# Kernel tuning notes

Hardware: AMD Instinct MI355X
Metric: run time of the kernel (lower is better)

The kernel has to match this reference:

```python
import jax, jax.numpy as jnp
import numpy as np

EPS = 1e-12  # matches torch F.normalize eps


def setup_inputs() -> dict:
    key = jax.random.key(0)
    k1, k2 = jax.random.split(key)
    N, D, K = 262144, 128, 512
    embeddings = jax.random.normal(k1, (N, D), dtype=jnp.float32)
    init_centroids = jax.random.normal(k2, (K, D), dtype=jnp.float32)
    return {"embeddings": embeddings, "init_centroids": init_centroids, "num_iters": 5}


def _kmeans_iter(centroids, embeddings, K):
    # [N, K] similarity, hard assignment by argmax (k-means E-step with dot-product metric)
    dots = jnp.matmul(embeddings, centroids.T)
    assign = jnp.argmax(dots, axis=1)  # [N] int32
    # M-step: per-cluster sum + counts (replaces CPU dict-of-lists + python loop)
    emb_sums = jax.ops.segment_sum(embeddings, assign, num_segments=K)  # [K, D]
    counts = jax.ops.segment_sum(jnp.ones(embeddings.shape[0], dtype=embeddings.dtype),
                                 assign, num_segments=K)  # [K]
    # only update clusters with members (mask = counts > 0), keep old centroid otherwise
    new_c = jnp.where(counts[:, None] > 0,
                      emb_sums / jnp.maximum(counts, 1.0)[:, None],
                      centroids)
    # F.normalize(dim=1, p=2) applied to ALL centroids
    norm = jnp.maximum(jnp.linalg.norm(new_c, axis=1, keepdims=True), EPS)
    return new_c / norm, assign


def reference(embeddings, init_centroids, num_iters):
    K = init_centroids.shape[0]
    centroids = init_centroids
    assign = jnp.zeros(embeddings.shape[0], dtype=jnp.int32)
    for _ in range(num_iters):  # small static iteration count (k-means iters)
        centroids, assign = _kmeans_iter(centroids, embeddings, K)
    return assign, centroids
```

## Files before the change

### kernel.cpp

```cpp
#include <hip/hip_runtime.h>

#define NN 262144
#define DD 128
#define KK 512
#define NITER 5

#define SKH 136

#define SE 132
#define SC 260
#define SS 129

#define DELTA 2e-3f

#define WS_A16_BYTES   (NN * 2)
#define WS_SUMS_OFF    (WS_A16_BYTES)
#define WS_CNTS_OFF    (WS_SUMS_OFF + 2048 * DD * 4)
#define WS_NEEDED      (WS_CNTS_OFF + 2048 * 4)
#define WS_CH_OFF      (WS_SUMS_OFF + NN)
#define WS_CL_OFF      (WS_CH_OFF + KK * DD * 2)

using s8    = __attribute__((ext_vector_type(8))) short;
using f32x4 = __attribute__((ext_vector_type(4))) float;

__device__ __forceinline__ unsigned f2bf(float x) {
    unsigned u = __float_as_uint(x);
    return (u + 0x7fffu + ((u >> 16) & 1u)) >> 16;
}

__device__ __forceinline__ void split4(float4 v, uint2& h, uint2& s) {
    unsigned hx = f2bf(v.x), hy = f2bf(v.y), hz = f2bf(v.z), hw = f2bf(v.w);
    float rx = v.x - __uint_as_float(hx << 16);
    float ry = v.y - __uint_as_float(hy << 16);
    float rz = v.z - __uint_as_float(hz << 16);
    float rw = v.w - __uint_as_float(hw << 16);
    unsigned lx = f2bf(rx), ly = f2bf(ry), lz = f2bf(rz), lw = f2bf(rw);
    h.x = hx | (hy << 16); h.y = hz | (hw << 16);
    s.x = lx | (ly << 16); s.y = lz | (lw << 16);
}

__global__ __launch_bounds__(256) void split_c_kernel(
    const float* __restrict__ C, unsigned short* __restrict__ CH,
    unsigned short* __restrict__ CL)
{
    int idx = blockIdx.x * 256 + threadIdx.x;
    int col = idx >> 5;
    int k4  = (idx & 31) << 2;
    float4 v = *(const float4*)&C[(size_t)col * DD + k4];
    uint2 h, s;
    split4(v, h, s);
    int group = (col >> 4) * 4 + (k4 >> 5);
    int inner = ((k4 >> 3) & 3) * 16 + (col & 15);
    int off   = group * 512 + inner * 8 + (k4 & 7);
    *(uint2*)&CH[off] = h;
    *(uint2*)&CL[off] = s;
}

__global__ __launch_bounds__(256, 2) void assign_kernel(
    const float* __restrict__ E,
    const unsigned short* __restrict__ CH, const unsigned short* __restrict__ CL,
    int* __restrict__ assignv, unsigned short* __restrict__ assign16,
    unsigned char* __restrict__ flags)
{
    __shared__ unsigned short lds[2 * 128 * SKH];
    unsigned short* EH = lds;
    unsigned short* EL = lds + 128 * SKH;

    const int tid = threadIdx.x;
    const int l   = tid & 63;
    const int wid = tid >> 6;
    const int wr  = wid >> 1;
    const int wc  = wid & 1;
    const int c   = l & 15;
    const int g   = l >> 4;
    const int r0  = blockIdx.x * 128;

#pragma unroll
    for (int it = 0; it < 16; ++it) {
        int idx = it * 256 + tid;
        int row = idx >> 5;
        int k4  = (idx & 31) << 2;
        float4 v = *(const float4*)&E[(size_t)(r0 + row) * DD + k4];
        uint2 h, s;
        split4(v, h, s);
        *(uint2*)&EH[row * SKH + k4] = h;
        *(uint2*)&EL[row * SKH + k4] = s;
    }
    __syncthreads();

    float bv[16], sv[16];
    int   bk[16];
#pragma unroll
    for (int i = 0; i < 16; ++i) { bv[i] = -3.4e38f; sv[i] = -3.4e38f; bk[i] = 0; }

    const int aoff0 = (wr * 64 + c) * SKH + g * 8;
    const int bbase = wc * 16 * 512 + l * 8;

    s8 bh[2][4], bl[2][4];
#pragma unroll
    for (int cf = 0; cf < 4; ++cf) {
        int off = bbase + (cf * 4) * 512;
        bh[0][cf] = *(const s8*)&CH[off];
        bl[0][cf] = *(const s8*)&CL[off];
    }

    f32x4 acc[4][4];

#pragma unroll
    for (int t = 0; t < 16; ++t) {
        const int cc  = t >> 2, kc = t & 3;
        const int cur = t & 1,  nxt = cur ^ 1;

        if (kc == 0) {
#pragma unroll
            for (int rf = 0; rf < 4; ++rf)
#pragma unroll
                for (int cf = 0; cf < 4; ++cf)
                    acc[rf][cf] = (f32x4){0.f, 0.f, 0.f, 0.f};
        }

        if (t < 15) {
            const int t1 = t + 1, cc1 = t1 >> 2, kc1 = t1 & 3;
#pragma unroll
            for (int cf = 0; cf < 4; ++cf) {
                int off = bbase + (cc1 * 32 + cf * 4 + kc1) * 512;
                bh[nxt][cf] = *(const s8*)&CH[off];
                bl[nxt][cf] = *(const s8*)&CL[off];
            }
        }

        s8 ah[4], al[4];
#pragma unroll
        for (int rf = 0; rf < 4; ++rf) {
            int off = aoff0 + rf * 16 * SKH + kc * 32;
            ah[rf] = *(const s8*)&EH[off];
            al[rf] = *(const s8*)&EL[off];
        }

#pragma unroll
        for (int rf = 0; rf < 4; ++rf)
#pragma unroll
            for (int cf = 0; cf < 4; ++cf) {
                acc[rf][cf] = __builtin_amdgcn_mfma_f32_16x16x32_bf16(
                    ah[rf], bh[cur][cf], acc[rf][cf], 0, 0, 0);
                acc[rf][cf] = __builtin_amdgcn_mfma_f32_16x16x32_bf16(
                    ah[rf], bl[cur][cf], acc[rf][cf], 0, 0, 0);
                acc[rf][cf] = __builtin_amdgcn_mfma_f32_16x16x32_bf16(
                    al[rf], bh[cur][cf], acc[rf][cf], 0, 0, 0);
            }

        if (kc == 3) {
            const int kbase = cc * 128 + wc * 64 + c;
#pragma unroll
            for (int rf = 0; rf < 4; ++rf)
#pragma unroll
                for (int i = 0; i < 4; ++i) {
                    const int sidx = rf * 4 + i;
#pragma unroll
                    for (int cf = 0; cf < 4; ++cf) {
                        float v = acc[rf][cf][i];
                        int  kg = kbase + cf * 16;
                        if (v > bv[sidx]) { sv[sidx] = bv[sidx]; bv[sidx] = v; bk[sidx] = kg; }
                        else              { sv[sidx] = fmaxf(sv[sidx], v); }
                    }
                }
        }
    }

#pragma unroll
    for (int s = 0; s < 16; ++s) {
        float v1 = bv[s], v2 = sv[s]; int k1 = bk[s];
#pragma unroll
        for (int m = 1; m <= 8; m <<= 1) {
            float ov = __shfl_xor(v1, m, 64);
            float os = __shfl_xor(v2, m, 64);
            int   ok = __shfl_xor(k1, m, 64);
            if (ov > v1) { v2 = fmaxf(v1, os); v1 = ov; k1 = ok; }
            else         { v2 = fmaxf(v2, ov); }
        }
        bv[s] = v1; sv[s] = v2; bk[s] = k1;
    }

    __syncthreads();
    float* mv = (float*)lds;
    int*   mk = (int*)lds + 256;
    float* ms = (float*)lds + 512;
    if (c == 0) {
#pragma unroll
        for (int rf = 0; rf < 4; ++rf)
#pragma unroll
            for (int i = 0; i < 4; ++i) {
                int row = wr * 64 + rf * 16 + g * 4 + i;
                mv[wc * 128 + row] = bv[rf * 4 + i];
                mk[wc * 128 + row] = bk[rf * 4 + i];
                ms[wc * 128 + row] = sv[rf * 4 + i];
            }
    }
    __syncthreads();
    if (tid < 128) {
        float v1 = mv[tid], v2 = ms[tid]; int k1 = mk[tid];
        float ov = mv[128 + tid], os = ms[128 + tid]; int ok = mk[128 + tid];
        if (ov > v1) { v2 = fmaxf(v1, os); v1 = ov; k1 = ok; }
        else         { v2 = fmaxf(v2, ov); }
        assignv[r0 + tid] = k1;
        assign16[r0 + tid] = (unsigned short)k1;
        flags[r0 + tid] = (v1 - v2 < DELTA) ? 1 : 0;
    }
}

__global__ __launch_bounds__(256) void rescue_kernel(
    const float* __restrict__ E, const float* __restrict__ C,
    const unsigned char* __restrict__ flags,
    int* __restrict__ assignv, unsigned short* __restrict__ assign16)
{
    __shared__ int   rows[128];
    __shared__ int   nf;
    __shared__ float ev[DD];
    __shared__ float rv[4];
    __shared__ int   rk[4];

    const int tid  = threadIdx.x;
    const int base = blockIdx.x * 128;

    if (tid == 0) nf = 0;
    __syncthreads();
    if (tid < 128 && flags[base + tid]) {
        int p = atomicAdd(&nf, 1);
        rows[p] = base + tid;
    }
    __syncthreads();
    const int n = nf;
    if (n == 0) return;

    for (int i = 0; i < n; ++i) {
        const int row = rows[i];
        if (tid < 32)
            *(float4*)&ev[tid * 4] = *(const float4*)&E[(size_t)row * DD + tid * 4];
        __syncthreads();

        float d0 = 0.f, d1 = 0.f;
        for (int q = 0; q < 32; ++q) {
            float4 e4 = *(const float4*)&ev[q * 4];
            float4 c0 = *(const float4*)&C[(size_t)tid * DD + q * 4];
            float4 c1 = *(const float4*)&C[(size_t)(tid + 256) * DD + q * 4];
            d0 = fmaf(e4.x, c0.x, d0); d0 = fmaf(e4.y, c0.y, d0);
            d0 = fmaf(e4.z, c0.z, d0); d0 = fmaf(e4.w, c0.w, d0);
            d1 = fmaf(e4.x, c1.x, d1); d1 = fmaf(e4.y, c1.y, d1);
            d1 = fmaf(e4.z, c1.z, d1); d1 = fmaf(e4.w, c1.w, d1);
        }
        float v = (d0 >= d1) ? d0 : d1;
        int   k = (d0 >= d1) ? tid : tid + 256;
#pragma unroll
        for (int m = 1; m <= 32; m <<= 1) {
            float ov = __shfl_xor(v, m, 64);
            int   ok = __shfl_xor(k, m, 64);
            if (ov > v || (ov == v && ok < k)) { v = ov; k = ok; }
        }
        if ((tid & 63) == 0) { rv[tid >> 6] = v; rk[tid >> 6] = k; }
        __syncthreads();
        if (tid == 0) {
            float bv2 = rv[0]; int bk2 = rk[0];
#pragma unroll
            for (int w = 1; w < 4; ++w)
                if (rv[w] > bv2 || (rv[w] == bv2 && rk[w] < bk2)) { bv2 = rv[w]; bk2 = rk[w]; }
            assignv[row] = bk2;
            assign16[row] = (unsigned short)bk2;
        }
        __syncthreads();
    }
}

__global__ __launch_bounds__(256, 2) void assign_valu_kernel(
    const float* __restrict__ E, const float* __restrict__ C,
    int* __restrict__ assignv, unsigned short* __restrict__ assign16)
{
    __shared__ float smem[32 * SE + 32 * SC];
    float* ET = smem;
    float* CT = smem + 32 * SE;
    float* sval = smem;
    int*   sidx = ((int*)smem) + 32 * SS;

    const int tid = threadIdx.x;
    const int tx  = tid & 31;
    const int ty  = tid >> 5;
    const int r0  = blockIdx.x * 128;

    float bbv = 0.f;
    int   bbk = 0;

    for (int chunk = 0; chunk < 2; ++chunk) {
        const int k0 = chunk * 256;
        float acc[16][8];
#pragma unroll
        for (int i = 0; i < 16; ++i)
#pragma unroll
            for (int j = 0; j < 8; ++j) acc[i][j] = 0.f;

        for (int sub = 0; sub < 4; ++sub) {
            const int d0 = sub * 32;
            __syncthreads();
#pragma unroll
            for (int it = 0; it < 4; ++it) {
                int idx = tid + it * 256;
                int r = idx >> 3, q = idx & 7;
                float4 v = *(const float4*)&E[(r0 + r) * DD + d0 + q * 4];
                ET[(q * 4 + 0) * SE + r] = v.x;
                ET[(q * 4 + 1) * SE + r] = v.y;
                ET[(q * 4 + 2) * SE + r] = v.z;
                ET[(q * 4 + 3) * SE + r] = v.w;
            }
#pragma unroll
            for (int it = 0; it < 8; ++it) {
                int idx = tid + it * 256;
                int k = idx >> 3, q = idx & 7;
                float4 v = *(const float4*)&C[(k0 + k) * DD + d0 + q * 4];
                CT[(q * 4 + 0) * SC + k] = v.x;
                CT[(q * 4 + 1) * SC + k] = v.y;
                CT[(q * 4 + 2) * SC + k] = v.z;
                CT[(q * 4 + 3) * SC + k] = v.w;
            }
            __syncthreads();
#pragma unroll 4
            for (int d = 0; d < 32; ++d) {
                float4 a0 = *(const float4*)&ET[d * SE + ty * 16];
                float4 a1 = *(const float4*)&ET[d * SE + ty * 16 + 4];
                float4 a2 = *(const float4*)&ET[d * SE + ty * 16 + 8];
                float4 a3 = *(const float4*)&ET[d * SE + ty * 16 + 12];
                float4 b0 = *(const float4*)&CT[d * SC + tx * 4];
                float4 b1 = *(const float4*)&CT[d * SC + 128 + tx * 4];
                float ra[16] = {a0.x, a0.y, a0.z, a0.w, a1.x, a1.y, a1.z, a1.w,
                                a2.x, a2.y, a2.z, a2.w, a3.x, a3.y, a3.z, a3.w};
                float rb[8]  = {b0.x, b0.y, b0.z, b0.w, b1.x, b1.y, b1.z, b1.w};
#pragma unroll
                for (int i = 0; i < 16; ++i)
#pragma unroll
                    for (int j = 0; j < 8; ++j)
                        acc[i][j] = fmaf(ra[i], rb[j], acc[i][j]);
            }
        }
        __syncthreads();

#pragma unroll
        for (int i = 0; i < 16; ++i) {
            float bv = acc[i][0]; int bj = 0;
#pragma unroll
            for (int j = 1; j < 8; ++j)
                if (acc[i][j] > bv) { bv = acc[i][j]; bj = j; }
            int row = ty * 16 + i;
            int gk = k0 + ((bj < 4) ? (tx * 4 + bj) : (128 + tx * 4 + (bj - 4)));
            sval[tx * SS + row] = bv;
            sidx[tx * SS + row] = gk;
        }
        __syncthreads();
        if (tid < 128) {
            float bv = sval[tid]; int bi = sidx[tid];
            for (int t = 1; t < 32; ++t) {
                float v = sval[t * SS + tid];
                int   x = sidx[t * SS + tid];
                if (v > bv || (v == bv && x < bi)) { bv = v; bi = x; }
            }
            if (chunk == 0 || bv > bbv || (bv == bbv && bi < bbk)) {
                bbv = bv; bbk = bi;
            }
        }
    }
    if (tid < 128) {
        assignv[r0 + tid] = bbk;
        if (assign16) assign16[r0 + tid] = (unsigned short)bbk;
    }
}

__global__ __launch_bounds__(256) void update_partial_kernel(
    const float* __restrict__ E, const unsigned short* __restrict__ assign16,
    float* __restrict__ ws_sums, int* __restrict__ ws_cnts)
{
    const int b   = blockIdx.x;
    const int k   = b >> 2;
    const int qtr = b & 3;

    __shared__ float acc[4][DD];
    __shared__ int   cnts[4];

    const int tid  = threadIdx.x;
    const int w    = tid >> 6;
    const int lane = tid & 63;

    float a0 = 0.f, a1 = 0.f;
    int cnt = 0;
    const int wbase = qtr * (NN / 4) + w * (NN / 16);

    for (int it = 0; it < (NN / 16) / 512; ++it) {
        const int off = wbase + it * 512;
        uint4 p = *(const uint4*)&assign16[off + lane * 8];
        unsigned v[4] = {p.x, p.y, p.z, p.w};
#pragma unroll
        for (int h = 0; h < 4; ++h) {
            int lo = (int)(v[h] & 0xffffu);
            int hi = (int)(v[h] >> 16);
            unsigned long long mlo = __ballot(lo == k);
            unsigned long long mhi = __ballot(hi == k);
            cnt += (int)__popcll(mlo) + (int)__popcll(mhi);
            while (mlo) {
                int b2 = __ffsll((long long)mlo) - 1; mlo &= mlo - 1;
                int row = off + b2 * 8 + h * 2;
                float2 e = *(const float2*)&E[(size_t)row * DD + lane * 2];
                a0 += e.x; a1 += e.y;
            }
            while (mhi) {
                int b2 = __ffsll((long long)mhi) - 1; mhi &= mhi - 1;
                int row = off + b2 * 8 + h * 2 + 1;
                float2 e = *(const float2*)&E[(size_t)row * DD + lane * 2];
                a0 += e.x; a1 += e.y;
            }
        }
    }
    acc[w][lane * 2]     = a0;
    acc[w][lane * 2 + 1] = a1;
    if (lane == 0) cnts[w] = cnt;
    __syncthreads();
    if (tid < DD)
        ws_sums[(size_t)b * DD + tid] = acc[0][tid] + acc[1][tid] + acc[2][tid] + acc[3][tid];
    if (tid == 0)
        ws_cnts[b] = cnts[0] + cnts[1] + cnts[2] + cnts[3];
}

__global__ __launch_bounds__(128) void update_combine_kernel(
    const float* __restrict__ ws_sums, const int* __restrict__ ws_cnts,
    float* __restrict__ C)
{
    const int k = blockIdx.x, t = threadIdx.x;
    __shared__ float red[2];
    const int w = t >> 6, lane = t & 63;

    float s = ws_sums[(size_t)(4 * k + 0) * DD + t]
            + ws_sums[(size_t)(4 * k + 1) * DD + t]
            + ws_sums[(size_t)(4 * k + 2) * DD + t]
            + ws_sums[(size_t)(4 * k + 3) * DD + t];
    int cnt = ws_cnts[4 * k] + ws_cnts[4 * k + 1] + ws_cnts[4 * k + 2] + ws_cnts[4 * k + 3];
    float m = (cnt > 0) ? s / (float)cnt : C[k * DD + t];

    float sq = m * m;
#pragma unroll
    for (int o = 32; o > 0; o >>= 1) sq += __shfl_down(sq, o, 64);
    if (lane == 0) red[w] = sq;
    __syncthreads();
    float nrm = fmaxf(sqrtf(red[0] + red[1]), 1e-12f);
    C[k * DD + t] = m / nrm;
}

__global__ __launch_bounds__(256) void update_kernel(
    const float* __restrict__ E, const int* __restrict__ assignv,
    float* __restrict__ C)
{
    const int k = blockIdx.x;
    __shared__ float acc[4][DD];
    __shared__ int   cnts[4];
    __shared__ float red[4];

    const int tid  = threadIdx.x;
    const int w    = tid >> 6;
    const int lane = tid & 63;

    float a0 = 0.f, a1 = 0.f;
    int cnt = 0;
    const int per_wave = NN / 4;
    const int base = w * per_wave;

    for (int it = 0; it < per_wave / 256; ++it) {
        const int off = base + it * 256;
        int4 as = *(const int4*)&assignv[off + lane * 4];
        int av[4] = {as.x, as.y, as.z, as.w};
#pragma unroll
        for (int ci = 0; ci < 4; ++ci) {
            unsigned long long m = __ballot(av[ci] == k);
            cnt += (int)__popcll(m);
            while (m) {
                int b = __ffsll((long long)m) - 1;
                m &= m - 1;
                int r = off + b * 4 + ci;
                float2 v = *(const float2*)&E[r * DD + lane * 2];
                a0 += v.x; a1 += v.y;
            }
        }
    }
    acc[w][lane * 2]     = a0;
    acc[w][lane * 2 + 1] = a1;
    if (lane == 0) cnts[w] = cnt;
    __syncthreads();

    float m = 0.f;
    const int ctot = cnts[0] + cnts[1] + cnts[2] + cnts[3];
    if (tid < DD) {
        float s = acc[0][tid] + acc[1][tid] + acc[2][tid] + acc[3][tid];
        m = (ctot > 0) ? s / (float)ctot : C[k * DD + tid];
    }
    float sq = m * m;
#pragma unroll
    for (int o = 32; o > 0; o >>= 1) sq += __shfl_down(sq, o, 64);
    if (lane == 0) red[w] = sq;
    __syncthreads();
    if (tid < DD) {
        float nrm = fmaxf(sqrtf(red[0] + red[1]), 1e-12f);
        C[k * DD + tid] = m / nrm;
    }
}

__global__ void finalize_kernel(float* __restrict__ out)
{
    int i = blockIdx.x * 256 + threadIdx.x;
    if (i < NN) {
        int a = ((const int*)out)[i];
        out[i] = (float)a;
    }
}

extern "C" void kernel_launch(void* const* d_in, const int* in_sizes, int n_in,
                              void* d_out, int out_size, void* d_ws, size_t ws_size,
                              hipStream_t stream)
{
    (void)in_sizes; (void)n_in; (void)out_size;

    const float* E  = (const float*)d_in[0];
    const float* C0 = (const float*)d_in[1];

    float* out     = (float*)d_out;
    float* C       = out + NN;
    int*   assignv = (int*)out;

    const bool fast = (ws_size >= (size_t)WS_NEEDED);
    unsigned short* assign16 = fast ? (unsigned short*)d_ws : nullptr;
    float* ws_sums = fast ? (float*)((char*)d_ws + WS_SUMS_OFF) : nullptr;
    int*   ws_cnts = fast ? (int*)((char*)d_ws + WS_CNTS_OFF) : nullptr;
    unsigned char* flags = fast ? (unsigned char*)d_ws + WS_SUMS_OFF : nullptr;
    unsigned short* CH = fast ? (unsigned short*)((char*)d_ws + WS_CH_OFF) : nullptr;
    unsigned short* CL = fast ? (unsigned short*)((char*)d_ws + WS_CL_OFF) : nullptr;

    hipMemcpyAsync(C, C0, (size_t)KK * DD * sizeof(float),
                   hipMemcpyDeviceToDevice, stream);

    for (int it = 0; it < NITER; ++it) {
        if (fast) {
            split_c_kernel<<<KK * DD / 4 / 256, 256, 0, stream>>>(C, CH, CL);
            assign_kernel<<<NN / 128, 256, 0, stream>>>(E, CH, CL, assignv, assign16, flags);
            rescue_kernel<<<NN / 128, 256, 0, stream>>>(E, C, flags, assignv, assign16);
            update_partial_kernel<<<2048, 256, 0, stream>>>(E, assign16, ws_sums, ws_cnts);
            update_combine_kernel<<<KK, 128, 0, stream>>>(ws_sums, ws_cnts, C);
        } else {
            assign_valu_kernel<<<NN / 128, 256, 0, stream>>>(E, C, assignv, nullptr);
            update_kernel<<<KK, 256, 0, stream>>>(E, assignv, C);
        }
    }
    finalize_kernel<<<(NN + 255) / 256, 256, 0, stream>>>(out);
}
```

Measured before the change: 1.475 ms.

## Pre-split embeddings into MFMA-fragment bf16 hi/lo layout once for all iterations

Adds a one-time kernel that splits the fp32 embeddings into bf16 high and low parts and stores them in a fragment-ordered layout. It also adds a matching centroid layout and a new assign kernel that loads MFMA operands straight from global memory, with no LDS staging, and computes the 3-product split-bf16 dot. The aim is to stop re-splitting E in every iteration and to remove LDS traffic from the assignment GEMM. The cost is a 128 MB workspace, and the path is only taken if the workspace is large enough, otherwise it falls back to the old path.

```diff
diff --git a/kernel.cpp b/kernel.cpp
--- a/kernel.cpp
+++ b/kernel.cpp
@@ -19,6 +19,10 @@
 #define WS_NEEDED      (WS_CNTS_OFF + 2048 * 4)
 #define WS_CH_OFF      (WS_SUMS_OFF + NN)
 #define WS_CL_OFF      (WS_CH_OFF + KK * DD * 2)
+#define WS_CB_OFF      (WS_SUMS_OFF + NN)
+#define WS_EAB_OFF     (WS_NEEDED)
+#define WS_EAB_BYTES   (4 * 16384 * 2 * 1024)
+#define WS_NEEDED2     (WS_EAB_OFF + WS_EAB_BYTES)
 
 using s8    = __attribute__((ext_vector_type(8))) short;
 using f32x4 = __attribute__((ext_vector_type(4))) float;
@@ -37,6 +41,171 @@
     unsigned lx = f2bf(rx), ly = f2bf(ry), lz = f2bf(rz), lw = f2bf(rw);
     h.x = hx | (hy << 16); h.y = hz | (hw << 16);
     s.x = lx | (ly << 16); s.y = lz | (lw << 16);
+}
+
+__global__ __launch_bounds__(256) void presplit_e_kernel(
+    const float* __restrict__ E, unsigned short* __restrict__ EAB)
+{
+    const int u   = blockIdx.x * 4 + (threadIdx.x >> 6);
+    const int l   = threadIdx.x & 63;
+    const int kc  = u >> 14;
+    const int grp = u & 16383;
+    const int row = grp * 16 + (l & 15);
+    const int k0  = kc * 32 + (l >> 4) * 8;
+    float4 v0 = *(const float4*)&E[(size_t)row * DD + k0];
+    float4 v1 = *(const float4*)&E[(size_t)row * DD + k0 + 4];
+    uint2 h0, s0, h1, s1;
+    split4(v0, h0, s0); split4(v1, h1, s1);
+    size_t base = (size_t)u * 2048 + l * 16;
+    *(uint2*)((char*)EAB + base)        = h0;
+    *(uint2*)((char*)EAB + base + 8)    = h1;
+    *(uint2*)((char*)EAB + base + 1024) = s0;
+    *(uint2*)((char*)EAB + base + 1032) = s1;
+}
+
+__global__ __launch_bounds__(256) void split_cb_kernel(
+    const float* __restrict__ C, unsigned short* __restrict__ CB)
+{
+    const int u   = blockIdx.x * 4 + (threadIdx.x >> 6);
+    const int l   = threadIdx.x & 63;
+    const int cc  = u >> 5;
+    const int kc  = (u >> 3) & 3;
+    const int wcf = u & 7;
+    const int col = cc * 128 + wcf * 16 + (l & 15);
+    const int k0  = kc * 32 + (l >> 4) * 8;
+    float4 v0 = *(const float4*)&C[(size_t)col * DD + k0];
+    float4 v1 = *(const float4*)&C[(size_t)col * DD + k0 + 4];
+    uint2 h0, s0, h1, s1;
+    split4(v0, h0, s0); split4(v1, h1, s1);
+    size_t base = (size_t)u * 2048 + l * 16;
+    *(uint2*)((char*)CB + base)        = h0;
+    *(uint2*)((char*)CB + base + 8)    = h1;
+    *(uint2*)((char*)CB + base + 1024) = s0;
+    *(uint2*)((char*)CB + base + 1032) = s1;
+}
+
+__global__ __launch_bounds__(256, 2) void assign_g_kernel(
+    const unsigned short* __restrict__ EAB, const unsigned short* __restrict__ CB,
+    int* __restrict__ assignv, unsigned short* __restrict__ assign16,
+    unsigned char* __restrict__ flags)
+{
+    __shared__ float smv[256];
+    __shared__ int   smk[256];
+    __shared__ float sms[256];
+
+    const int tid = threadIdx.x;
+    const int l   = tid & 63;
+    const int wid = tid >> 6;
+    const int wr  = wid >> 1;
+    const int wc  = wid & 1;
+    const int c   = l & 15;
+    const int g   = l >> 4;
+    const int r0  = blockIdx.x * 128;
+
+    float bv[16], sv[16];
+    int   bk[16];
+#pragma unroll
+    for (int i = 0; i < 16; ++i) { bv[i] = -3.4e38f; sv[i] = -3.4e38f; bk[i] = 0; }
+
+    const int voffA  = (blockIdx.x * 8 + wr * 4) * 2048 + l * 16 + 4096;
+    const int voffB0 = wc * 8192 + l * 16 + 4096;
+    const char* Ab = (const char*)EAB;
+    const char* Bb = (const char*)CB;
+
+    f32x4 acc[4][4];
+
+#pragma unroll
+    for (int t = 0; t < 16; ++t) {
+        const int cc = t >> 2, kc = t & 3;
+
+        if (kc == 0) {
+#pragma unroll
+            for (int rf = 0; rf < 4; ++rf)
+#pragma unroll
+                for (int cf = 0; cf < 4; ++cf)
+                    acc[rf][cf] = (f32x4){0.f, 0.f, 0.f, 0.f};
+        }
+
+        const char* Akc = Ab + (size_t)kc * 33554432;
+        const int   vB  = voffB0 + t * 16384;
+
+        s8 ah[4], al[4], bh[4], bl[4];
+#pragma unroll
+        for (int rf = 0; rf < 4; ++rf) {
+            ah[rf] = *(const s8*)(Akc + voffA + (rf * 2048 - 4096));
+            al[rf] = *(const s8*)(Akc + voffA + (rf * 2048 + 1024 - 4096));
+        }
+#pragma unroll
+        for (int cf = 0; cf < 4; ++cf) {
+            bh[cf] = *(const s8*)(Bb + vB + (cf * 2048 - 4096));
+            bl[cf] = *(const s8*)(Bb + vB + (cf * 2048 + 1024 - 4096));
+        }
+
+#pragma unroll
+        for (int rf = 0; rf < 4; ++rf)
+#pragma unroll
+            for (int cf = 0; cf < 4; ++cf) {
+                acc[rf][cf] = __builtin_amdgcn_mfma_f32_16x16x32_bf16(
+                    ah[rf], bh[cf], acc[rf][cf], 0, 0, 0);
+                acc[rf][cf] = __builtin_amdgcn_mfma_f32_16x16x32_bf16(
+                    ah[rf], bl[cf], acc[rf][cf], 0, 0, 0);
+                acc[rf][cf] = __builtin_amdgcn_mfma_f32_16x16x32_bf16(
+                    al[rf], bh[cf], acc[rf][cf], 0, 0, 0);
+            }
+
+        if (kc == 3) {
+            const int kbase = cc * 128 + wc * 64 + c;
+#pragma unroll
+            for (int rf = 0; rf < 4; ++rf)
+#pragma unroll
+                for (int i = 0; i < 4; ++i) {
+                    const int sidx = rf * 4 + i;
+#pragma unroll
+                    for (int cf = 0; cf < 4; ++cf) {
+                        float v = acc[rf][cf][i];
+                        int  kg = kbase + cf * 16;
+                        if (v > bv[sidx]) { sv[sidx] = bv[sidx]; bv[sidx] = v; bk[sidx] = kg; }
+                        else              { sv[sidx] = fmaxf(sv[sidx], v); }
+                    }
+                }
+        }
+    }
+
+#pragma unroll
+    for (int s = 0; s < 16; ++s) {
+        float v1 = bv[s], v2 = sv[s]; int k1 = bk[s];
+#pragma unroll
+        for (int m = 1; m <= 8; m <<= 1) {
+            float ov = __shfl_xor(v1, m, 64);
+            float os = __shfl_xor(v2, m, 64);
+            int   ok = __shfl_xor(k1, m, 64);
+            if (ov > v1) { v2 = fmaxf(v1, os); v1 = ov; k1 = ok; }
+            else         { v2 = fmaxf(v2, ov); }
+        }
+        bv[s] = v1; sv[s] = v2; bk[s] = k1;
+    }
+
+    if (c == 0) {
+#pragma unroll
+        for (int rf = 0; rf < 4; ++rf)
+#pragma unroll
+            for (int i = 0; i < 4; ++i) {
+                int row = wr * 64 + rf * 16 + g * 4 + i;
+                smv[wc * 128 + row] = bv[rf * 4 + i];
+                smk[wc * 128 + row] = bk[rf * 4 + i];
+                sms[wc * 128 + row] = sv[rf * 4 + i];
+            }
+    }
+    __syncthreads();
+    if (tid < 128) {
+        float v1 = smv[tid], v2 = sms[tid]; int k1 = smk[tid];
+        float ov = smv[128 + tid], os = sms[128 + tid]; int ok = smk[128 + tid];
+        if (ov > v1) { v2 = fmaxf(v1, os); v1 = ov; k1 = ok; }
+        else         { v2 = fmaxf(v2, ov); }
+        assignv[r0 + tid] = k1;
+        assign16[r0 + tid] = (unsigned short)k1;
+        flags[r0 + tid] = (v1 - v2 < DELTA) ? 1 : 0;
+    }
 }
 
 __global__ __launch_bounds__(256) void split_c_kernel(
@@ -527,19 +696,31 @@
     float* C       = out + NN;
     int*   assignv = (int*)out;
 
-    const bool fast = (ws_size >= (size_t)WS_NEEDED);
+    const bool fast  = (ws_size >= (size_t)WS_NEEDED);
+    const bool fast2 = (ws_size >= (size_t)WS_NEEDED2);
     unsigned short* assign16 = fast ? (unsigned short*)d_ws : nullptr;
     float* ws_sums = fast ? (float*)((char*)d_ws + WS_SUMS_OFF) : nullptr;
     int*   ws_cnts = fast ? (int*)((char*)d_ws + WS_CNTS_OFF) : nullptr;
     unsigned char* flags = fast ? (unsigned char*)d_ws + WS_SUMS_OFF : nullptr;
     unsigned short* CH = fast ? (unsigned short*)((char*)d_ws + WS_CH_OFF) : nullptr;
     unsigned short* CL = fast ? (unsigned short*)((char*)d_ws + WS_CL_OFF) : nullptr;
+    unsigned short* CB = fast ? (unsigned short*)((char*)d_ws + WS_CB_OFF) : nullptr;
+    unsigned short* EAB = fast2 ? (unsigned short*)((char*)d_ws + WS_EAB_OFF) : nullptr;
 
     hipMemcpyAsync(C, C0, (size_t)KK * DD * sizeof(float),
                    hipMemcpyDeviceToDevice, stream);
 
+    if (fast2)
+        presplit_e_kernel<<<16384, 256, 0, stream>>>(E, EAB);
+
     for (int it = 0; it < NITER; ++it) {
-        if (fast) {
+        if (fast2) {
+            split_cb_kernel<<<32, 256, 0, stream>>>(C, CB);
+            assign_g_kernel<<<NN / 128, 256, 0, stream>>>(EAB, CB, assignv, assign16, flags);
+            rescue_kernel<<<NN / 128, 256, 0, stream>>>(E, C, flags, assignv, assign16);
+            update_partial_kernel<<<2048, 256, 0, stream>>>(E, assign16, ws_sums, ws_cnts);
+            update_combine_kernel<<<KK, 128, 0, stream>>>(ws_sums, ws_cnts, C);
+        } else if (fast) {
             split_c_kernel<<<KK * DD / 4 / 256, 256, 0, stream>>>(C, CH, CL);
             assign_kernel<<<NN / 128, 256, 0, stream>>>(E, CH, CL, assignv, assign16, flags);
             rescue_kernel<<<NN / 128, 256, 0, stream>>>(E, C, flags, assignv, assign16);
```

New measurement: 1.863 ms. +26.3%, slower.

## Pre-split embeddings to bf16 hi/lo once and use 32x32x16 MFMA assign kernel

Applied to the files above, without the earlier changes.

Embeddings are split into bf16 high/low halves once, before the k-means loop, into a workspace buffer, so the per-iteration assign kernel no longer reconverts fp32 embeddings. A new assign kernel uses 32x32x16 bf16 MFMA tiles with a matching centroid layout, three-product split precision, and tracks best and second-best scores to flag near-ties for rescue. This costs an extra 128 MB workspace plus one upfront conversion pass, and the new path runs only when the workspace is large enough.

```diff
diff --git a/kernel.cpp b/kernel.cpp
--- a/kernel.cpp
+++ b/kernel.cpp
@@ -19,9 +19,13 @@
 #define WS_NEEDED      (WS_CNTS_OFF + 2048 * 4)
 #define WS_CH_OFF      (WS_SUMS_OFF + NN)
 #define WS_CL_OFF      (WS_CH_OFF + KK * DD * 2)
-
-using s8    = __attribute__((ext_vector_type(8))) short;
-using f32x4 = __attribute__((ext_vector_type(4))) float;
+#define WS_EH2_OFF     (WS_NEEDED)
+#define WS_EL2_OFF     (WS_EH2_OFF + NN * DD * 2)
+#define WS_NEEDED2     (WS_EL2_OFF + NN * DD * 2)
+
+using s8     = __attribute__((ext_vector_type(8))) short;
+using f32x4  = __attribute__((ext_vector_type(4))) float;
+using f32x16 = __attribute__((ext_vector_type(16))) float;
 
 __device__ __forceinline__ unsigned f2bf(float x) {
     unsigned u = __float_as_uint(x);
@@ -37,6 +41,141 @@
     unsigned lx = f2bf(rx), ly = f2bf(ry), lz = f2bf(rz), lw = f2bf(rw);
     h.x = hx | (hy << 16); h.y = hz | (hw << 16);
     s.x = lx | (ly << 16); s.y = lz | (lw << 16);
+}
+
+__global__ __launch_bounds__(256) void presplit_e2_kernel(
+    const float* __restrict__ E, unsigned short* __restrict__ EH2,
+    unsigned short* __restrict__ EL2)
+{
+    const size_t j = (size_t)blockIdx.x * 256 + threadIdx.x;
+    float4 v0 = *(const float4*)&E[j * 8];
+    float4 v1 = *(const float4*)&E[j * 8 + 4];
+    uint2 h0, s0, h1, s1;
+    split4(v0, h0, s0); split4(v1, h1, s1);
+    *(uint2*)((char*)EH2 + j * 16)     = h0;
+    *(uint2*)((char*)EH2 + j * 16 + 8) = h1;
+    *(uint2*)((char*)EL2 + j * 16)     = s0;
+    *(uint2*)((char*)EL2 + j * 16 + 8) = s1;
+}
+
+__global__ __launch_bounds__(256) void split_c3_kernel(
+    const float* __restrict__ C, unsigned short* __restrict__ CH,
+    unsigned short* __restrict__ CL)
+{
+    int idx = blockIdx.x * 256 + threadIdx.x;
+    int col = idx >> 5;
+    int k4  = (idx & 31) << 2;
+    float4 v = *(const float4*)&C[(size_t)col * DD + k4];
+    uint2 h, s;
+    split4(v, h, s);
+    int unit = (col >> 5) * 8 + (k4 >> 4);
+    int lane = (col & 31) + ((k4 >> 3) & 1) * 32;
+    int off  = unit * 512 + lane * 8 + (k4 & 7);
+    *(uint2*)&CH[off] = h;
+    *(uint2*)&CL[off] = s;
+}
+
+__global__ __launch_bounds__(256, 2) void assign3_kernel(
+    const unsigned short* __restrict__ EH2, const unsigned short* __restrict__ EL2,
+    const unsigned short* __restrict__ CH, const unsigned short* __restrict__ CL,
+    int* __restrict__ assignv, unsigned short* __restrict__ assign16,
+    unsigned char* __restrict__ flags)
+{
+    __shared__ unsigned short lds[2 * 128 * SKH];
+    unsigned short* EH = lds;
+    unsigned short* EL = lds + 128 * SKH;
+
+    const int tid = threadIdx.x;
+    const int l   = tid & 63;
+    const int wid = tid >> 6;
+    const int j   = l & 31;
+    const int h   = l >> 5;
+    const int r0  = blockIdx.x * 128;
+
+    {
+        const char* srcH = (const char*)EH2 + (size_t)r0 * 256;
+        const char* srcL = (const char*)EL2 + (size_t)r0 * 256;
+#pragma unroll
+        for (int it = 0; it < 8; ++it) {
+            int jj = it * 256 + tid;
+            int row = jj >> 4, k16 = jj & 15;
+            uint4 hh = *(const uint4*)(srcH + (size_t)jj * 16);
+            uint4 ss = *(const uint4*)(srcL + (size_t)jj * 16);
+            *(uint4*)((char*)&EH[row * SKH] + k16 * 16) = hh;
+            *(uint4*)((char*)&EL[row * SKH] + k16 * 16) = ss;
+        }
+    }
+    __syncthreads();
+
+    float bv[16], sv[16];
+    int   bk[16];
+#pragma unroll
+    for (int i = 0; i < 16; ++i) { bv[i] = -3.4e38f; sv[i] = -3.4e38f; bk[i] = 0; }
+
+    const int aoff0 = (wid * 32 + j) * SKH + h * 8;
+    const int boff0 = l * 8;
+
+#pragma unroll
+    for (int cc = 0; cc < 4; ++cc) {
+        f32x16 acc[4];
+#pragma unroll
+        for (int cf = 0; cf < 4; ++cf)
+#pragma unroll
+            for (int r = 0; r < 16; ++r) acc[cf][r] = 0.f;
+
+#pragma unroll
+        for (int ks = 0; ks < 8; ++ks) {
+            s8 ah = *(const s8*)&EH[aoff0 + ks * 16];
+            s8 al = *(const s8*)&EL[aoff0 + ks * 16];
+#pragma unroll
+            for (int cf = 0; cf < 4; ++cf) {
+                const int unit = (cc * 4 + cf) * 8 + ks;
+                s8 bh = *(const s8*)&CH[unit * 512 + boff0];
+                s8 bl = *(const s8*)&CL[unit * 512 + boff0];
+                acc[cf] = __builtin_amdgcn_mfma_f32_32x32x16_bf16(
+                    ah, bh, acc[cf], 0, 0, 0);
+                acc[cf] = __builtin_amdgcn_mfma_f32_32x32x16_bf16(
+                    ah, bl, acc[cf], 0, 0, 0);
+                acc[cf] = __builtin_amdgcn_mfma_f32_32x32x16_bf16(
+                    al, bh, acc[cf], 0, 0, 0);
+            }
+        }
+
+#pragma unroll
+        for (int cf = 0; cf < 4; ++cf) {
+            const int kg = cc * 128 + cf * 32 + j;
+#pragma unroll
+            for (int r = 0; r < 16; ++r) {
+                float v = acc[cf][r];
+                if (v > bv[r]) { sv[r] = bv[r]; bv[r] = v; bk[r] = kg; }
+                else           { sv[r] = fmaxf(sv[r], v); }
+            }
+        }
+    }
+
+#pragma unroll
+    for (int r = 0; r < 16; ++r) {
+        float v1 = bv[r], v2 = sv[r]; int k1 = bk[r];
+#pragma unroll
+        for (int m = 1; m <= 16; m <<= 1) {
+            float ov = __shfl_xor(v1, m, 64);
+            float os = __shfl_xor(v2, m, 64);
+            int   ok = __shfl_xor(k1, m, 64);
+            if (ov > v1) { v2 = fmaxf(v1, os); v1 = ov; k1 = ok; }
+            else         { v2 = fmaxf(v2, ov); }
+        }
+        bv[r] = v1; sv[r] = v2; bk[r] = k1;
+    }
+
+#pragma unroll
+    for (int r = 0; r < 16; ++r) {
+        if (j == r) {
+            int rowg = r0 + wid * 32 + (r & 3) + 8 * (r >> 2) + 4 * h;
+            assignv[rowg]  = bk[r];
+            assign16[rowg] = (unsigned short)bk[r];
+            flags[rowg]    = (bv[r] - sv[r] < DELTA) ? 1 : 0;
+        }
+    }
 }
 
 __global__ __launch_bounds__(256) void split_c_kernel(
@@ -527,19 +666,32 @@
     float* C       = out + NN;
     int*   assignv = (int*)out;
 
-    const bool fast = (ws_size >= (size_t)WS_NEEDED);
+    const bool fast  = (ws_size >= (size_t)WS_NEEDED);
+    const bool fast2 = (ws_size >= (size_t)WS_NEEDED2);
     unsigned short* assign16 = fast ? (unsigned short*)d_ws : nullptr;
     float* ws_sums = fast ? (float*)((char*)d_ws + WS_SUMS_OFF) : nullptr;
     int*   ws_cnts = fast ? (int*)((char*)d_ws + WS_CNTS_OFF) : nullptr;
     unsigned char* flags = fast ? (unsigned char*)d_ws + WS_SUMS_OFF : nullptr;
     unsigned short* CH = fast ? (unsigned short*)((char*)d_ws + WS_CH_OFF) : nullptr;
     unsigned short* CL = fast ? (unsigned short*)((char*)d_ws + WS_CL_OFF) : nullptr;
+    unsigned short* EH2 = fast2 ? (unsigned short*)((char*)d_ws + WS_EH2_OFF) : nullptr;
+    unsigned short* EL2 = fast2 ? (unsigned short*)((char*)d_ws + WS_EL2_OFF) : nullptr;
 
     hipMemcpyAsync(C, C0, (size_t)KK * DD * sizeof(float),
                    hipMemcpyDeviceToDevice, stream);
 
+    if (fast2)
+        presplit_e2_kernel<<<NN * DD / 8 / 256, 256, 0, stream>>>(E, EH2, EL2);
+
     for (int it = 0; it < NITER; ++it) {
-        if (fast) {
+        if (fast2) {
+            split_c3_kernel<<<KK * DD / 4 / 256, 256, 0, stream>>>(C, CH, CL);
+            assign3_kernel<<<NN / 128, 256, 0, stream>>>(EH2, EL2, CH, CL,
+                                                         assignv, assign16, flags);
+            rescue_kernel<<<NN / 128, 256, 0, stream>>>(E, C, flags, assignv, assign16);
+            update_partial_kernel<<<2048, 256, 0, stream>>>(E, assign16, ws_sums, ws_cnts);
+            update_combine_kernel<<<KK, 128, 0, stream>>>(ws_sums, ws_cnts, C);
+        } else if (fast) {
             split_c_kernel<<<KK * DD / 4 / 256, 256, 0, stream>>>(C, CH, CL);
             assign_kernel<<<NN / 128, 256, 0, stream>>>(E, CH, CL, assignv, assign16, flags);
             rescue_kernel<<<NN / 128, 256, 0, stream>>>(E, C, flags, assignv, assign16);
```

After: 1.642 ms. +11.3%, slower.
